# Optimization experiments

Hardware: AMD Instinct MI355X
Metric: run time of the kernel (lower is better)

Reference implementation:

```python
import jax, jax.numpy as jnp
import numpy as np

B, T, D = 2, 2048, 1024
H = 16
DH = D // H


def setup_inputs() -> dict:
    key = jax.random.key(0)
    ks = jax.random.split(key, 6)
    s = 1.0 / np.sqrt(D)
    return {
        "input_emb": jax.random.normal(ks[0], (B, T, D), dtype=jnp.float32),
        "W_key": jax.random.normal(ks[1], (D, D), dtype=jnp.float32) * s,
        "W_query": jax.random.normal(ks[2], (D, D), dtype=jnp.float32) * s,
        "W_value": jax.random.normal(ks[3], (D, D), dtype=jnp.float32) * s,
        "W_out": jax.random.normal(ks[4], (D, D), dtype=jnp.float32) * s,
        "b_out": jnp.zeros((D,), dtype=jnp.float32),
    }


def reference(input_emb, W_key, W_query, W_value, W_out, b_out):
    b, t, _ = input_emb.shape
    # projections (no bias on K/Q/V, matching bias_on=False)
    k = (input_emb @ W_key).reshape(b, t, H, DH).transpose(0, 2, 1, 3)    # [b,h,t,dh]
    q = (input_emb @ W_query).reshape(b, t, H, DH).transpose(0, 2, 1, 3)
    v = (input_emb @ W_value).reshape(b, t, H, DH).transpose(0, 2, 1, 3)
    # NOTE: source computes K @ Q^T (not Q @ K^T) — reproduce faithfully.
    scores = jnp.einsum("bhid,bhjd->bhij", k, q) / jnp.sqrt(jnp.float32(DH))
    mask = jnp.triu(jnp.ones((t, t), dtype=bool), k=1)                    # True where j > i
    scores = jnp.where(mask, -jnp.inf, scores)
    attn = jax.nn.softmax(scores, axis=-1)                                # softmax over j (query axis)
    ctx = jnp.einsum("bhij,bhjd->bhid", attn, v)                          # [b,h,t,dh]
    ctx = ctx.transpose(0, 2, 1, 3).reshape(b, t, H * DH)                 # [b,t,d]
    return ctx @ W_out + b_out
```

## Files before the change

### kernel.cpp

```cpp
#include <hip/hip_runtime.h>
#include <cstdint>
#include <cstddef>

#define T_SEQ 2048
#define DMODEL 1024
#define NHEAD 16
#define DHEAD 64
#define BATCH 2
#define MROWS (BATCH * T_SEQ)

typedef __attribute__((ext_vector_type(8))) short bf16x8;
typedef __attribute__((ext_vector_type(4))) float f32x4;
typedef unsigned int u32;

__device__ __forceinline__ unsigned short f2bf(float f) {
  u32 u = __float_as_uint(f);
  u32 r = (u + 0x7FFFu + ((u >> 16) & 1u)) >> 16;
  return (unsigned short)r;
}

__device__ __forceinline__ u32 cvtpk(float a, float b) {
  u32 r;
  asm("v_cvt_pk_bf16_f32 %0, %1, %2" : "=v"(r) : "v"(a), "v"(b));
  return r;
}

__device__ __forceinline__ void gl_lds16(const unsigned short* g, unsigned short* l) {
  __builtin_amdgcn_global_load_lds(
      (const __attribute__((address_space(1))) u32*)g,
      (__attribute__((address_space(3))) u32*)l, 16, 0, 0);
}

__global__ void k_cvt(const float* __restrict__ src, unsigned short* __restrict__ dst, int n) {
  int i = (blockIdx.x * 256 + threadIdx.x) * 4;
  if (i + 3 < n) {
    float4 v = *reinterpret_cast<const float4*>(src + i);
    ushort4 o;
    o.x = f2bf(v.x); o.y = f2bf(v.y); o.z = f2bf(v.z); o.w = f2bf(v.w);
    *reinterpret_cast<ushort4*>(dst + i) = o;
  }
}

__global__ void k_tc4(const float* __restrict__ W0, const float* __restrict__ W1,
                      const float* __restrict__ W2, const float* __restrict__ W3,
                      unsigned short* __restrict__ T0, unsigned short* __restrict__ T1,
                      unsigned short* __restrict__ T2, unsigned short* __restrict__ T3) {
  const int z = blockIdx.z;
  const float* W = (z == 0) ? W0 : (z == 1) ? W1 : (z == 2) ? W2 : W3;
  unsigned short* Wt = (z == 0) ? T0 : (z == 1) ? T1 : (z == 2) ? T2 : T3;
  __shared__ float tile[32][33];
  const int c0 = blockIdx.x * 32, r0 = blockIdx.y * 32;
  const int tx = threadIdx.x & 31, ty = threadIdx.x >> 5;
#pragma unroll
  for (int i = ty; i < 32; i += 8)
    tile[i][tx] = W[(size_t)(r0 + i) * DMODEL + c0 + tx];
  __syncthreads();
#pragma unroll
  for (int i = ty; i < 32; i += 8)
    Wt[(size_t)(c0 + i) * DMODEL + r0 + tx] = f2bf(tile[tx][i]);
}

__global__ __launch_bounds__(256, 2)
void k_gemm_qkv(const unsigned short* __restrict__ Xb,
                const unsigned short* __restrict__ Wkt,
                const unsigned short* __restrict__ Wqt,
                const unsigned short* __restrict__ Wvt,
                unsigned short* __restrict__ Qr,
                unsigned short* __restrict__ Kr,
                unsigned short* __restrict__ Vt)
{
  __shared__ __align__(16) unsigned short As[128 * 32];
  __shared__ __align__(16) unsigned short Bs[128 * 32];
  const int z = blockIdx.z;
  const unsigned short* Bt = (z == 0) ? Wkt : (z == 1) ? Wqt : Wvt;

  const int tid = threadIdx.x;
  const int lane = tid & 63, w = tid >> 6;
  const int wr = w >> 1, wc = w & 1;
  const int l15 = lane & 15, l4 = lane >> 4;
  const int m0 = blockIdx.y * 128, n0 = blockIdx.x * 128;

  f32x4 acc[4][4] = {};

  for (int k0 = 0; k0 < DMODEL; k0 += 32) {
#pragma unroll
    for (int i = 0; i < 2; ++i) {
      int c = i * 256 + tid;
      int row = c >> 2, cc = c & 3;
      gl_lds16(Xb + (size_t)(m0 + row) * DMODEL + k0 + cc * 8, As + c * 8);
      gl_lds16(Bt + (size_t)(n0 + row) * DMODEL + k0 + cc * 8, Bs + c * 8);
    }
    __syncthreads();
    bf16x8 af[4], bfr[4];
#pragma unroll
    for (int mi = 0; mi < 4; ++mi)
      af[mi] = *reinterpret_cast<const bf16x8*>(As + (wr * 64 + mi * 16 + l15) * 32 + l4 * 8);
#pragma unroll
    for (int ni = 0; ni < 4; ++ni)
      bfr[ni] = *reinterpret_cast<const bf16x8*>(Bs + (wc * 64 + ni * 16 + l15) * 32 + l4 * 8);
#pragma unroll
    for (int mi = 0; mi < 4; ++mi)
#pragma unroll
      for (int ni = 0; ni < 4; ++ni)
        acc[mi][ni] = __builtin_amdgcn_mfma_f32_16x16x32_bf16(af[mi], bfr[ni], acc[mi][ni], 0, 0, 0);
    __syncthreads();
  }

  if (z < 2) {
    unsigned short* C = (z == 0) ? Qr : Kr;
#pragma unroll
    for (int mi = 0; mi < 4; ++mi)
#pragma unroll
      for (int ni = 0; ni < 4; ++ni) {
        const int col = n0 + wc * 64 + ni * 16 + l15;
        const int rowb = m0 + wr * 64 + mi * 16 + l4 * 4;
#pragma unroll
        for (int r = 0; r < 4; ++r)
          C[(size_t)(rowb + r) * DMODEL + col] = f2bf(acc[mi][ni][r]);
      }
  } else {
#pragma unroll
    for (int mi = 0; mi < 4; ++mi)
#pragma unroll
      for (int ni = 0; ni < 4; ++ni) {
        const int col = n0 + wc * 64 + ni * 16 + l15;
        const int h = col >> 6, dh = col & 63;
        const int rowb = m0 + wr * 64 + mi * 16 + l4 * 4;
        const int b = rowb >> 11, t = rowb & (T_SEQ - 1);
        const int tl = t & 63;
        const int tp = (t & ~63) | (tl & 32) | ((tl & 12) << 1) | ((tl & 16) >> 2);
        unsigned short* p = Vt + ((size_t)(b * NHEAD + h) * DHEAD + dh) * T_SEQ + tp;
        ushort4 pkv;
        pkv.x = f2bf(acc[mi][ni][0]); pkv.y = f2bf(acc[mi][ni][1]);
        pkv.z = f2bf(acc[mi][ni][2]); pkv.w = f2bf(acc[mi][ni][3]);
        *reinterpret_cast<ushort4*>(p) = pkv;
      }
  }
}

__global__ __launch_bounds__(512, 2)
void k_attn(const unsigned short* __restrict__ Qr,
            const unsigned short* __restrict__ Kr,
            const unsigned short* __restrict__ Vp,
            unsigned short* __restrict__ ctx)
{
  __shared__ __align__(16) char lds[49152];
  const int tid = threadIdx.x;
  const int lane = tid & 63, w = tid >> 6;
  const int l15 = lane & 15, l4 = lane >> 4;

  const int x = blockIdx.x;
  const int xcd = x & 7, idx = x >> 3;
  const int bh = xcd + 8 * (idx & 3);
  const int cpair = idx >> 2;
  const int b = bh >> 4, h = bh & 15;

  const unsigned short* Qbase = Qr + (size_t)b * T_SEQ * DMODEL + h * DHEAD;
  const unsigned short* Kbase = Kr + (size_t)b * T_SEQ * DMODEL + h * DHEAD;
  const unsigned short* Vbase = Vp + (size_t)bh * DHEAD * T_SEQ;
  unsigned short* obase = ctx + (size_t)b * T_SEQ * DMODEL + h * DHEAD;

  const float SC = 0.18033688011112042f;

  for (int half = 0; half < 2; ++half) {
    const int c = half ? (15 - cpair) : cpair;
    const int q0b = c * 128;
    const int q0w = q0b + w * 16;
    const int NT = 2 * c + 2;
    const int ntw = ((q0w + 15) >> 6) + 1;

    bf16x8 qf[2];
#pragma unroll
    for (int ks = 0; ks < 2; ++ks)
      qf[ks] = *reinterpret_cast<const bf16x8*>(
          Qbase + (size_t)(q0w + l15) * DMODEL + ks * 32 + l4 * 8);

    __builtin_amdgcn_sched_barrier(0);
    __builtin_amdgcn_s_barrier();
    __builtin_amdgcn_sched_barrier(0);
#pragma unroll
    for (int pt = 0; pt < 2; ++pt) {
      unsigned short* Ks = (unsigned short*)(lds + pt * 8192);
      unsigned short* Vs = (unsigned short*)(lds + 24576 + pt * 8192);
      const int kvn = pt * 64;
      {
        const int cc = tid, row = cc >> 3, cb = cc & 7;
        const int colE = (cb ^ (row & 7)) << 3;
        gl_lds16(Kbase + (size_t)(kvn + row) * DMODEL + colE, Ks + cc * 8);
        gl_lds16(Vbase + (size_t)row * T_SEQ + kvn + colE, Vs + cc * 8);
      }
    }

    f32x4 O[4] = {};
    float mM = -INFINITY, lS = 0.f;

    for (int t = 0; t < NT; ++t) {
      const int kv0 = t * 64;
      const int buf = t % 3;
      const char* Ks = lds + buf * 8192;
      const char* Vs = lds + 24576 + buf * 8192;

      __builtin_amdgcn_sched_barrier(0);
      if (t + 1 < NT) {
        asm volatile("s_waitcnt vmcnt(2)" ::: "memory");
      } else {
        asm volatile("s_waitcnt vmcnt(0)" ::: "memory");
      }
      __builtin_amdgcn_sched_barrier(0);
      __builtin_amdgcn_s_barrier();
      __builtin_amdgcn_sched_barrier(0);

      if (t + 2 < NT) {
        const int nb = (t + 2) % 3;
        unsigned short* Kn = (unsigned short*)(lds + nb * 8192);
        unsigned short* Vn = (unsigned short*)(lds + 24576 + nb * 8192);
        const int kvn = kv0 + 128;
        const int cc = tid, row = cc >> 3, cb = cc & 7;
        const int colE = (cb ^ (row & 7)) << 3;
        gl_lds16(Kbase + (size_t)(kvn + row) * DMODEL + colE, Kn + cc * 8);
        gl_lds16(Vbase + (size_t)row * T_SEQ + kvn + colE, Vn + cc * 8);
      }
      __builtin_amdgcn_sched_barrier(0);

      if (t < ntw) {
        const bool maskt = (kv0 + 63 > q0w);
        int nlim = maskt ? (((q0w + 15 - kv0) >> 4) + 1) : 4;
        if (nlim > 4) nlim = 4;
        const int hklim = maskt ? ((nlim + 1) >> 1) : 2;

        f32x4 S[4] = {};
        __builtin_amdgcn_s_setprio(1);
#pragma unroll
        for (int ni = 0; ni < 4; ++ni) {
          if (ni < nlim) {
            const int row = ni * 16 + l15;
            const int sw = (row & 7) << 4;
            const bf16x8 k0 = *reinterpret_cast<const bf16x8*>(Ks + row * 128 + ((l4 * 16) ^ sw));
            const bf16x8 k1 = *reinterpret_cast<const bf16x8*>(Ks + row * 128 + ((64 + l4 * 16) ^ sw));
            S[ni] = __builtin_amdgcn_mfma_f32_16x16x32_bf16(k0, qf[0], S[ni], 0, 0, 0);
            S[ni] = __builtin_amdgcn_mfma_f32_16x16x32_bf16(k1, qf[1], S[ni], 0, 0, 0);
          }
        }
        __builtin_amdgcn_s_setprio(0);

        bf16x8 vf[4][2];
#pragma unroll
        for (int hk = 0; hk < 2; ++hk)
          if (hk < hklim)
#pragma unroll
            for (int df = 0; df < 4; ++df) {
              const int row = df * 16 + l15;
              const int sw = (row & 7) << 4;
              vf[df][hk] = *reinterpret_cast<const bf16x8*>(
                  Vs + row * 128 + ((hk * 64 + l4 * 16) ^ sw));
            }

        if (maskt) {
          const int q = q0w + l15;
#pragma unroll
          for (int ni = 0; ni < 4; ++ni)
#pragma unroll
            for (int r = 0; r < 4; ++r)
              if (kv0 + ni * 16 + l4 * 4 + r > q) S[ni][r] = -INFINITY;
        }

        float mx = fmaxf(fmaxf(S[0][0], S[0][1]), fmaxf(S[0][2], S[0][3]));
#pragma unroll
        for (int ni = 1; ni < 4; ++ni)
          mx = fmaxf(mx, fmaxf(fmaxf(S[ni][0], S[ni][1]), fmaxf(S[ni][2], S[ni][3])));
        mx = fmaxf(mx, __shfl_xor(mx, 16));
        mx = fmaxf(mx, __shfl_xor(mx, 32));
        const float pmax = mx * SC;
        if (!__all(pmax <= mM + 8.f)) {
          const float mn = fmaxf(mM, pmax);
          const float a = exp2f(mM - mn);
          mM = mn;
          lS *= a;
#pragma unroll
          for (int df = 0; df < 4; ++df) {
            O[df][0] *= a; O[df][1] *= a; O[df][2] *= a; O[df][3] *= a;
          }
        }
        u32 pk[8];
        float ps = 0.f;
#pragma unroll
        for (int ni = 0; ni < 4; ++ni) {
          const float p0 = exp2f(fmaf(S[ni][0], SC, -mM));
          const float p1 = exp2f(fmaf(S[ni][1], SC, -mM));
          const float p2 = exp2f(fmaf(S[ni][2], SC, -mM));
          const float p3 = exp2f(fmaf(S[ni][3], SC, -mM));
          ps += (p0 + p1) + (p2 + p3);
          pk[ni * 2]     = cvtpk(p0, p1);
          pk[ni * 2 + 1] = cvtpk(p2, p3);
        }
        ps += __shfl_xor(ps, 16);
        ps += __shfl_xor(ps, 32);
        lS += ps;

        __builtin_amdgcn_s_setprio(1);
#pragma unroll
        for (int hk = 0; hk < 2; ++hk)
          if (hk < hklim) {
            union { u32 u4[4]; bf16x8 v8; } pu;
            pu.u4[0] = pk[hk * 4 + 0]; pu.u4[1] = pk[hk * 4 + 1];
            pu.u4[2] = pk[hk * 4 + 2]; pu.u4[3] = pk[hk * 4 + 3];
#pragma unroll
            for (int df = 0; df < 4; ++df)
              O[df] = __builtin_amdgcn_mfma_f32_16x16x32_bf16(vf[df][hk], pu.v8, O[df], 0, 0, 0);
          }
        __builtin_amdgcn_s_setprio(0);
      }
      __builtin_amdgcn_sched_barrier(0);
    }

    {
      const float rinv = 1.0f / lS;
      const int q = q0w + l15;
#pragma unroll
      for (int df = 0; df < 4; ++df) {
        ushort4 o;
        o.x = f2bf(O[df][0] * rinv);
        o.y = f2bf(O[df][1] * rinv);
        o.z = f2bf(O[df][2] * rinv);
        o.w = f2bf(O[df][3] * rinv);
        *reinterpret_cast<ushort4*>(obase + (size_t)q * DMODEL + df * 16 + l4 * 4) = o;
      }
    }
  }
}

__global__ __launch_bounds__(256, 2)
void k_gemm_out(const unsigned short* __restrict__ Ab,
                const unsigned short* __restrict__ Bt,
                const float* __restrict__ bias,
                float* __restrict__ C)
{
  __shared__ __align__(16) unsigned short As[128 * 32];
  __shared__ __align__(16) unsigned short Bs[128 * 32];
  const int tid = threadIdx.x;
  const int lane = tid & 63, w = tid >> 6;
  const int wr = w >> 1, wc = w & 1;
  const int l15 = lane & 15, l4 = lane >> 4;
  const int m0 = blockIdx.y * 128, n0 = blockIdx.x * 128;

  f32x4 acc[4][4] = {};

  for (int k0 = 0; k0 < DMODEL; k0 += 32) {
#pragma unroll
    for (int i = 0; i < 2; ++i) {
      int c = i * 256 + tid;
      int row = c >> 2, cc = c & 3;
      gl_lds16(Ab + (size_t)(m0 + row) * DMODEL + k0 + cc * 8, As + c * 8);
      gl_lds16(Bt + (size_t)(n0 + row) * DMODEL + k0 + cc * 8, Bs + c * 8);
    }
    __syncthreads();
    bf16x8 af[4], bfr[4];
#pragma unroll
    for (int mi = 0; mi < 4; ++mi)
      af[mi] = *reinterpret_cast<const bf16x8*>(As + (wr * 64 + mi * 16 + l15) * 32 + l4 * 8);
#pragma unroll
    for (int ni = 0; ni < 4; ++ni)
      bfr[ni] = *reinterpret_cast<const bf16x8*>(Bs + (wc * 64 + ni * 16 + l15) * 32 + l4 * 8);
#pragma unroll
    for (int mi = 0; mi < 4; ++mi)
#pragma unroll
      for (int ni = 0; ni < 4; ++ni)
        acc[mi][ni] = __builtin_amdgcn_mfma_f32_16x16x32_bf16(af[mi], bfr[ni], acc[mi][ni], 0, 0, 0);
    __syncthreads();
  }

#pragma unroll
  for (int mi = 0; mi < 4; ++mi)
#pragma unroll
    for (int ni = 0; ni < 4; ++ni) {
      const int col = n0 + wc * 64 + ni * 16 + l15;
      const float bv = bias[col];
      const int rowb = m0 + wr * 64 + mi * 16 + l4 * 4;
#pragma unroll
      for (int r = 0; r < 4; ++r)
        C[(size_t)(rowb + r) * DMODEL + col] = acc[mi][ni][r] + bv;
    }
}

extern "C" void kernel_launch(void* const* d_in, const int* in_sizes, int n_in,
                              void* d_out, int out_size, void* d_ws, size_t ws_size,
                              hipStream_t stream) {
  const float* X  = (const float*)d_in[0];
  const float* Wk = (const float*)d_in[1];
  const float* Wq = (const float*)d_in[2];
  const float* Wv = (const float*)d_in[3];
  const float* Wo = (const float*)d_in[4];
  const float* bo = (const float*)d_in[5];
  float* out = (float*)d_out;

  char* ws = (char*)d_ws;
  const size_t MB = 1024 * 1024;
  unsigned short* Xb  = (unsigned short*)(ws + 0 * MB);
  unsigned short* Wkt = (unsigned short*)(ws + 8 * MB);
  unsigned short* Wqt = (unsigned short*)(ws + 10 * MB);
  unsigned short* Wvt = (unsigned short*)(ws + 12 * MB);
  unsigned short* Wot = (unsigned short*)(ws + 14 * MB);
  unsigned short* Qr  = (unsigned short*)(ws + 16 * MB);
  unsigned short* Kr  = (unsigned short*)(ws + 24 * MB);
  unsigned short* Vt  = (unsigned short*)(ws + 32 * MB);
  unsigned short* Ctx = (unsigned short*)(ws + 40 * MB);

  k_cvt<<<4096, 256, 0, stream>>>(X, Xb, MROWS * DMODEL);
  k_tc4<<<dim3(32, 32, 4), 256, 0, stream>>>(Wk, Wq, Wv, Wo, Wkt, Wqt, Wvt, Wot);

  k_gemm_qkv<<<dim3(8, 32, 3), 256, 0, stream>>>(Xb, Wkt, Wqt, Wvt, Qr, Kr, Vt);
  k_attn<<<dim3(256), 512, 0, stream>>>(Qr, Kr, Vt, Ctx);
  k_gemm_out<<<dim3(8, 32), 256, 0, stream>>>(Ctx, Wot, bo, out);
}
```

Baseline: 126.5 us.

## Process 128-key groups per iteration with double-buffered LDS in attention

The attention loop now handles two 64-key sub-tiles per iteration (128 keys), with one online-softmax max/rescale per group. LDS staging moves from a triple buffer of 64-row K/V tiles to a double buffer of 128-row groups, which halves the number of block barriers and softmax reductions. In exchange, LDS grows to 64KB and register pressure rises (S[2][4], vf[2][4][2]). The loads now wait on vmcnt(0), which removes the partial overlap the old triple buffer allowed and may reduce occupancy at launch_bounds(512,2).

```diff
diff --git a/kernel.cpp b/kernel.cpp
--- a/kernel.cpp
+++ b/kernel.cpp
@@ -144,7 +144,7 @@
             const unsigned short* __restrict__ Vp,
             unsigned short* __restrict__ ctx)
 {
-  __shared__ __align__(16) char lds[49152];
+  __shared__ __align__(16) char lds[65536];
   const int tid = threadIdx.x;
   const int lane = tid & 63, w = tid >> 6;
   const int l15 = lane & 15, l4 = lane >> 4;
@@ -161,13 +161,14 @@
   unsigned short* obase = ctx + (size_t)b * T_SEQ * DMODEL + h * DHEAD;
 
   const float SC = 0.18033688011112042f;
+  const int srow = tid >> 3, scb = tid & 7;
+  const int scolE = (scb ^ (srow & 7)) << 3;
 
   for (int half = 0; half < 2; ++half) {
     const int c = half ? (15 - cpair) : cpair;
-    const int q0b = c * 128;
-    const int q0w = q0b + w * 16;
-    const int NT = 2 * c + 2;
-    const int ntw = ((q0w + 15) >> 6) + 1;
+    const int q0w = c * 128 + w * 16;
+    const int NG = c + 1;
+    const int lastT = q0w >> 6;
 
     bf16x8 qf[2];
 #pragma unroll
@@ -178,96 +179,114 @@
     __builtin_amdgcn_sched_barrier(0);
     __builtin_amdgcn_s_barrier();
     __builtin_amdgcn_sched_barrier(0);
-#pragma unroll
-    for (int pt = 0; pt < 2; ++pt) {
-      unsigned short* Ks = (unsigned short*)(lds + pt * 8192);
-      unsigned short* Vs = (unsigned short*)(lds + 24576 + pt * 8192);
-      const int kvn = pt * 64;
-      {
-        const int cc = tid, row = cc >> 3, cb = cc & 7;
-        const int colE = (cb ^ (row & 7)) << 3;
-        gl_lds16(Kbase + (size_t)(kvn + row) * DMODEL + colE, Ks + cc * 8);
-        gl_lds16(Vbase + (size_t)row * T_SEQ + kvn + colE, Vs + cc * 8);
-      }
+    {
+      unsigned short* Ks = (unsigned short*)(lds);
+      unsigned short* Vs = (unsigned short*)(lds + 32768);
+      gl_lds16(Kbase + (size_t)srow * DMODEL + scolE, Ks + tid * 8);
+      gl_lds16(Kbase + (size_t)(64 + srow) * DMODEL + scolE, Ks + 4096 + tid * 8);
+      gl_lds16(Vbase + (size_t)srow * T_SEQ + scolE, Vs + tid * 8);
+      gl_lds16(Vbase + (size_t)srow * T_SEQ + 64 + scolE, Vs + 4096 + tid * 8);
     }
 
     f32x4 O[4] = {};
     float mM = -INFINITY, lS = 0.f;
 
-    for (int t = 0; t < NT; ++t) {
-      const int kv0 = t * 64;
-      const int buf = t % 3;
-      const char* Ks = lds + buf * 8192;
-      const char* Vs = lds + 24576 + buf * 8192;
+    for (int g = 0; g < NG; ++g) {
+      const int kv0 = g * 128;
+      const int gp = g & 1;
+      const char* Kg = lds + gp * 16384;
+      const char* Vg = lds + 32768 + gp * 16384;
 
       __builtin_amdgcn_sched_barrier(0);
-      if (t + 1 < NT) {
-        asm volatile("s_waitcnt vmcnt(2)" ::: "memory");
-      } else {
-        asm volatile("s_waitcnt vmcnt(0)" ::: "memory");
-      }
+      asm volatile("s_waitcnt vmcnt(0)" ::: "memory");
       __builtin_amdgcn_sched_barrier(0);
       __builtin_amdgcn_s_barrier();
       __builtin_amdgcn_sched_barrier(0);
 
-      if (t + 2 < NT) {
-        const int nb = (t + 2) % 3;
-        unsigned short* Kn = (unsigned short*)(lds + nb * 8192);
-        unsigned short* Vn = (unsigned short*)(lds + 24576 + nb * 8192);
+      if (g + 1 < NG) {
+        unsigned short* Kn = (unsigned short*)(lds + (gp ^ 1) * 16384);
+        unsigned short* Vn = (unsigned short*)(lds + 32768 + (gp ^ 1) * 16384);
         const int kvn = kv0 + 128;
-        const int cc = tid, row = cc >> 3, cb = cc & 7;
-        const int colE = (cb ^ (row & 7)) << 3;
-        gl_lds16(Kbase + (size_t)(kvn + row) * DMODEL + colE, Kn + cc * 8);
-        gl_lds16(Vbase + (size_t)row * T_SEQ + kvn + colE, Vn + cc * 8);
+        gl_lds16(Kbase + (size_t)(kvn + srow) * DMODEL + scolE, Kn + tid * 8);
+        gl_lds16(Kbase + (size_t)(kvn + 64 + srow) * DMODEL + scolE, Kn + 4096 + tid * 8);
+        gl_lds16(Vbase + (size_t)srow * T_SEQ + kvn + scolE, Vn + tid * 8);
+        gl_lds16(Vbase + (size_t)srow * T_SEQ + kvn + 64 + scolE, Vn + 4096 + tid * 8);
       }
       __builtin_amdgcn_sched_barrier(0);
 
-      if (t < ntw) {
-        const bool maskt = (kv0 + 63 > q0w);
-        int nlim = maskt ? (((q0w + 15 - kv0) >> 4) + 1) : 4;
-        if (nlim > 4) nlim = 4;
-        const int hklim = maskt ? ((nlim + 1) >> 1) : 2;
-
-        f32x4 S[4] = {};
+      if (2 * g <= lastT) {
+        const bool a1 = (2 * g + 1 <= lastT);
+        int nlv[2]; bool mkv[2];
+#pragma unroll
+        for (int st = 0; st < 2; ++st) {
+          const int kvst = kv0 + st * 64;
+          mkv[st] = (kvst + 63 > q0w);
+          int nl = 4;
+          if (mkv[st]) { nl = ((q0w + 15 - kvst) >> 4) + 1; if (nl > 4) nl = 4; if (nl < 0) nl = 0; }
+          nlv[st] = nl;
+        }
+
+        f32x4 S[2][4] = {};
         __builtin_amdgcn_s_setprio(1);
 #pragma unroll
-        for (int ni = 0; ni < 4; ++ni) {
-          if (ni < nlim) {
-            const int row = ni * 16 + l15;
-            const int sw = (row & 7) << 4;
-            const bf16x8 k0 = *reinterpret_cast<const bf16x8*>(Ks + row * 128 + ((l4 * 16) ^ sw));
-            const bf16x8 k1 = *reinterpret_cast<const bf16x8*>(Ks + row * 128 + ((64 + l4 * 16) ^ sw));
-            S[ni] = __builtin_amdgcn_mfma_f32_16x16x32_bf16(k0, qf[0], S[ni], 0, 0, 0);
-            S[ni] = __builtin_amdgcn_mfma_f32_16x16x32_bf16(k1, qf[1], S[ni], 0, 0, 0);
+        for (int st = 0; st < 2; ++st) {
+          if (st == 1 && !a1) break;
+          const char* Ks = Kg + st * 8192;
+#pragma unroll
+          for (int ni = 0; ni < 4; ++ni) {
+            if (ni < nlv[st]) {
+              const int row = ni * 16 + l15;
+              const int sw = (row & 7) << 4;
+              const bf16x8 k0 = *reinterpret_cast<const bf16x8*>(Ks + row * 128 + ((l4 * 16) ^ sw));
+              const bf16x8 k1 = *reinterpret_cast<const bf16x8*>(Ks + row * 128 + ((64 + l4 * 16) ^ sw));
+              S[st][ni] = __builtin_amdgcn_mfma_f32_16x16x32_bf16(k0, qf[0], S[st][ni], 0, 0, 0);
+              S[st][ni] = __builtin_amdgcn_mfma_f32_16x16x32_bf16(k1, qf[1], S[st][ni], 0, 0, 0);
+            }
           }
         }
         __builtin_amdgcn_s_setprio(0);
 
-        bf16x8 vf[4][2];
-#pragma unroll
-        for (int hk = 0; hk < 2; ++hk)
-          if (hk < hklim)
-#pragma unroll
-            for (int df = 0; df < 4; ++df) {
-              const int row = df * 16 + l15;
-              const int sw = (row & 7) << 4;
-              vf[df][hk] = *reinterpret_cast<const bf16x8*>(
-                  Vs + row * 128 + ((hk * 64 + l4 * 16) ^ sw));
-            }
-
-        if (maskt) {
-          const int q = q0w + l15;
+        bf16x8 vf[2][4][2];
+#pragma unroll
+        for (int st = 0; st < 2; ++st) {
+          if (st == 1 && !a1) break;
+          const char* Vs = Vg + st * 8192;
+          const int hkl = mkv[st] ? ((nlv[st] + 1) >> 1) : 2;
+#pragma unroll
+          for (int hk = 0; hk < 2; ++hk)
+            if (hk < hkl)
+#pragma unroll
+              for (int df = 0; df < 4; ++df) {
+                const int row = df * 16 + l15;
+                const int sw = (row & 7) << 4;
+                vf[st][df][hk] = *reinterpret_cast<const bf16x8*>(
+                    Vs + row * 128 + ((hk * 64 + l4 * 16) ^ sw));
+              }
+        }
+
+#pragma unroll
+        for (int st = 0; st < 2; ++st) {
+          if (st == 1 && !a1) break;
+          if (mkv[st]) {
+            const int q = q0w + l15;
+            const int kvst = kv0 + st * 64;
+#pragma unroll
+            for (int ni = 0; ni < 4; ++ni)
+#pragma unroll
+              for (int r = 0; r < 4; ++r)
+                if (kvst + ni * 16 + l4 * 4 + r > q) S[st][ni][r] = -INFINITY;
+          }
+        }
+
+        float mx = fmaxf(fmaxf(S[0][0][0], S[0][0][1]), fmaxf(S[0][0][2], S[0][0][3]));
+#pragma unroll
+        for (int ni = 1; ni < 4; ++ni)
+          mx = fmaxf(mx, fmaxf(fmaxf(S[0][ni][0], S[0][ni][1]), fmaxf(S[0][ni][2], S[0][ni][3])));
+        if (a1) {
 #pragma unroll
           for (int ni = 0; ni < 4; ++ni)
-#pragma unroll
-            for (int r = 0; r < 4; ++r)
-              if (kv0 + ni * 16 + l4 * 4 + r > q) S[ni][r] = -INFINITY;
-        }
-
-        float mx = fmaxf(fmaxf(S[0][0], S[0][1]), fmaxf(S[0][2], S[0][3]));
-#pragma unroll
-        for (int ni = 1; ni < 4; ++ni)
-          mx = fmaxf(mx, fmaxf(fmaxf(S[ni][0], S[ni][1]), fmaxf(S[ni][2], S[ni][3])));
+            mx = fmaxf(mx, fmaxf(fmaxf(S[1][ni][0], S[1][ni][1]), fmaxf(S[1][ni][2], S[1][ni][3])));
+        }
         mx = fmaxf(mx, __shfl_xor(mx, 16));
         mx = fmaxf(mx, __shfl_xor(mx, 32));
         const float pmax = mx * SC;
@@ -281,17 +300,21 @@
             O[df][0] *= a; O[df][1] *= a; O[df][2] *= a; O[df][3] *= a;
           }
         }
-        u32 pk[8];
+        u32 pk[2][8];
         float ps = 0.f;
 #pragma unroll
-        for (int ni = 0; ni < 4; ++ni) {
-          const float p0 = exp2f(fmaf(S[ni][0], SC, -mM));
-          const float p1 = exp2f(fmaf(S[ni][1], SC, -mM));
-          const float p2 = exp2f(fmaf(S[ni][2], SC, -mM));
-          const float p3 = exp2f(fmaf(S[ni][3], SC, -mM));
-          ps += (p0 + p1) + (p2 + p3);
-          pk[ni * 2]     = cvtpk(p0, p1);
-          pk[ni * 2 + 1] = cvtpk(p2, p3);
+        for (int st = 0; st < 2; ++st) {
+          if (st == 1 && !a1) break;
+#pragma unroll
+          for (int ni = 0; ni < 4; ++ni) {
+            const float p0 = exp2f(fmaf(S[st][ni][0], SC, -mM));
+            const float p1 = exp2f(fmaf(S[st][ni][1], SC, -mM));
+            const float p2 = exp2f(fmaf(S[st][ni][2], SC, -mM));
+            const float p3 = exp2f(fmaf(S[st][ni][3], SC, -mM));
+            ps += (p0 + p1) + (p2 + p3);
+            pk[st][ni * 2]     = cvtpk(p0, p1);
+            pk[st][ni * 2 + 1] = cvtpk(p2, p3);
+          }
         }
         ps += __shfl_xor(ps, 16);
         ps += __shfl_xor(ps, 32);
@@ -299,15 +322,20 @@
 
         __builtin_amdgcn_s_setprio(1);
 #pragma unroll
-        for (int hk = 0; hk < 2; ++hk)
-          if (hk < hklim) {
-            union { u32 u4[4]; bf16x8 v8; } pu;
-            pu.u4[0] = pk[hk * 4 + 0]; pu.u4[1] = pk[hk * 4 + 1];
-            pu.u4[2] = pk[hk * 4 + 2]; pu.u4[3] = pk[hk * 4 + 3];
-#pragma unroll
-            for (int df = 0; df < 4; ++df)
-              O[df] = __builtin_amdgcn_mfma_f32_16x16x32_bf16(vf[df][hk], pu.v8, O[df], 0, 0, 0);
-          }
+        for (int st = 0; st < 2; ++st) {
+          if (st == 1 && !a1) break;
+          const int hkl = mkv[st] ? ((nlv[st] + 1) >> 1) : 2;
+#pragma unroll
+          for (int hk = 0; hk < 2; ++hk)
+            if (hk < hkl) {
+              union { u32 u4[4]; bf16x8 v8; } pu;
+              pu.u4[0] = pk[st][hk * 4 + 0]; pu.u4[1] = pk[st][hk * 4 + 1];
+              pu.u4[2] = pk[st][hk * 4 + 2]; pu.u4[3] = pk[st][hk * 4 + 3];
+#pragma unroll
+              for (int df = 0; df < 4; ++df)
+                O[df] = __builtin_amdgcn_mfma_f32_16x16x32_bf16(vf[st][df][hk], pu.v8, O[df], 0, 0, 0);
+            }
+        }
         __builtin_amdgcn_s_setprio(0);
       }
       __builtin_amdgcn_sched_barrier(0);
```

After: 118.8 us. 6.0% less time.
